# Performance work log

Measured on AMD Instinct MI355X. Metric: run time of the kernel, lower is better.

The kernel has to match this reference:

```python
import jax, jax.numpy as jnp
import numpy as np

N0, N1, N2 = 60000, 30000, 15000
E1, E2 = 960000, 480000
G, D, C = 2000, 400, 20
S0, S1, S2 = 1000, 1500, 2000  # gene index slice boundaries (shared/human/mouse)
EPS = 1e-5


def setup_inputs() -> dict:
    key = jax.random.key(0)
    ks = jax.random.split(key, 30)
    def lin(k, o, i):
        return (jax.random.normal(k, (o, i), jnp.float32) / np.sqrt(i)).astype(jnp.float32)
    inp = {}
    inp['x'] = jax.random.normal(ks[0], (N0, G), jnp.float32)
    inp['w_all'] = jax.random.uniform(ks[1], (E1 + E2, 1), jnp.float32)
    inp['W_sh'] = lin(ks[2], D, 1000); inp['b_sh'] = 0.01 * jax.random.normal(ks[3], (D,), jnp.float32)
    inp['W_hu'] = lin(ks[4], D, 500);  inp['b_hu'] = 0.01 * jax.random.normal(ks[5], (D,), jnp.float32)
    inp['W_mo'] = lin(ks[6], D, 500);  inp['b_mo'] = 0.01 * jax.random.normal(ks[7], (D,), jnp.float32)
    inp['Wn1'] = lin(ks[8], D, D);     inp['bn1'] = 0.01 * jax.random.normal(ks[9], (D,), jnp.float32)
    inp['Wn2'] = lin(ks[10], D, D);    inp['bn2'] = 0.01 * jax.random.normal(ks[11], (D,), jnp.float32)
    inp['W_lin'] = lin(ks[12], C, D);  inp['b_lin'] = 0.01 * jax.random.normal(ks[13], (C,), jnp.float32)
    inp['Wd1'] = lin(ks[14], 50, D);   inp['bd1'] = 0.01 * jax.random.normal(ks[15], (50,), jnp.float32)
    inp['gamma'] = jnp.ones((50,), jnp.float32)
    inp['beta'] = jnp.zeros((50,), jnp.float32)
    inp['Wd2'] = lin(ks[16], 2, 50);   inp['bd2'] = 0.01 * jax.random.normal(ks[17], (2,), jnp.float32)
    inp['src1'] = jax.random.randint(ks[18], (E1,), 0, N0)
    inp['dst1'] = jax.random.randint(ks[19], (E1,), 0, N1)
    inp['eid1'] = jax.random.randint(ks[20], (E1,), 0, E1 + E2)
    inp['src2'] = jax.random.randint(ks[21], (E2,), 0, N1)
    inp['dst2'] = jax.random.randint(ks[22], (E2,), 0, N2)
    inp['eid2'] = jax.random.randint(ks[23], (E2,), 0, E1 + E2)
    return inp


@jax.custom_vjp
def grad_reverse(x):
    return x

def _gr_fwd(x):
    return x, None

def _gr_bwd(_, g):
    return (-g,)  # ReverseLayerF with alpha=1

grad_reverse.defvjp(_gr_fwd, _gr_bwd)


def _gnn_layer(h_src, n_dst, src, dst, w_e, W, b):
    # weighted message gather-sum + degree-normalized self-combine (GNNConv)
    h_dst = h_src[:n_dst]
    m = h_src[src] * w_e                                   # [E, D]
    neigh = jax.ops.segment_sum(m, dst, num_segments=n_dst)
    deg = jax.ops.segment_sum(jnp.ones(dst.shape, h_src.dtype), dst, num_segments=n_dst)
    h_neigh = (neigh + h_dst) / (deg[:, None] + 1.0)
    return h_neigh @ W.T + b


def reference(x, w_all, W_sh, b_sh, W_hu, b_hu, W_mo, b_mo, Wn1, bn1, Wn2, bn2,
              W_lin, b_lin, Wd1, bd1, gamma, beta, Wd2, bd2,
              src1, dst1, eid1, src2, dst2, eid2):
    # one-hot selection matmuls == column slices of x, then three embeddings summed (FineGrainedLayerF)
    h = ((x[:, :S0] @ W_sh.T + b_sh)
         + (x[:, S0:S1] @ W_hu.T + b_hu)
         + (x[:, S1:S2] @ W_mo.T + b_mo))
    h1 = _gnn_layer(h, N1, src1, dst1, w_all[eid1], Wn1, bn1)
    h2 = _gnn_layer(h1, N2, src2, dst2, w_all[eid2], Wn2, bn2)
    h_x = h2 @ W_lin.T + b_lin
    # domain classifier on gradient-reversed features (BatchNorm1d in training mode)
    d = grad_reverse(h2) @ Wd1.T + bd1
    mu = jnp.mean(d, axis=0)
    var = jnp.var(d, axis=0)
    d = (d - mu) / jnp.sqrt(var + EPS) * gamma + beta
    d = jax.nn.relu(d)
    domain_x = d @ Wd2.T + bd2
    return (h_x, domain_x)
```

## Files before the change

### kernel.cpp

```cpp
#include <hip/hip_runtime.h>
#include <stdint.h>
#include <stddef.h>

typedef short bf16x8 __attribute__((ext_vector_type(8)));
typedef unsigned short ushort8 __attribute__((ext_vector_type(8)));
typedef unsigned short usv4 __attribute__((ext_vector_type(4)));
typedef float f32x4 __attribute__((ext_vector_type(4)));

__device__ __forceinline__ unsigned short f2bf(float f) {
  union { float f; unsigned int u; } v; v.f = f;
  unsigned int r = v.u + 0x7FFFu + ((v.u >> 16) & 1u);
  return (unsigned short)(r >> 16);
}
__device__ __forceinline__ float bf2f(unsigned short u) {
  union { unsigned int u; float f; } v; v.u = ((unsigned int)u) << 16; return v.f;
}

#define PAD 96

__global__ void prep_frag(
    const float* __restrict__ Wsh, const float* __restrict__ Whu, const float* __restrict__ Wmo,
    const float* __restrict__ Wn1, const float* __restrict__ Wn2,
    const float* __restrict__ Wlin, const float* __restrict__ Wd1,
    unsigned short* __restrict__ WCf, unsigned short* __restrict__ WN1f,
    unsigned short* __restrict__ WN2f, unsigned short* __restrict__ WHf,
    const float* __restrict__ bsh, const float* __restrict__ bhu, const float* __restrict__ bmo,
    const float* __restrict__ blin, const float* __restrict__ bd1,
    float* __restrict__ b3, float* __restrict__ bhead)
{
  const int NB_FRAG = 6784;
  const int bid = blockIdx.x;
  const int tid = threadIdx.x;
  if (bid < NB_FRAG) {
    const int s0 = 64 * 16384, s1 = s0 + 14 * 16384, s2 = s1 + 14 * 16384;
    int idx = bid * 256 + tid;
    int mode, rel;
    unsigned short* out;
    if (idx < s0)      { mode = 0; rel = idx;      out = WCf;  }
    else if (idx < s1) { mode = 1; rel = idx - s0; out = WN1f; }
    else if (idx < s2) { mode = 3; rel = idx - s1; out = WN2f; }
    else               { mode = 2; rel = idx - s2; out = WHf;  }
    int t = rel >> 14;
    int rem = rel & 16383;
    int e = rem & 7;
    int chunk = rem >> 3;
    int lane = chunk & 63;
    int g = chunk >> 6;
    int col = g * 16 + (lane & 15);
    int k = t * 32 + ((lane >> 4) << 3) + e;
    float v = 0.f;
    if (mode == 0) {
      if (col < 400 && k < 2000) {
        if (k < 1000)      v = Wsh[col * 1000 + k];
        else if (k < 1500) v = Whu[col * 500 + (k - 1000)];
        else               v = Wmo[col * 500 + (k - 1500)];
      }
    } else if (mode == 1) {
      if (col < 400 && k < 400) v = Wn1[col * 400 + k];
    } else if (mode == 3) {
      if (col < 400 && k < 400) v = Wn2[col * 400 + k];
    } else {
      if (k < 400) {
        if (col < 20)      v = Wlin[col * 400 + k];
        else if (col < 70) v = Wd1[(col - 20) * 400 + k];
      }
    }
    out[rel] = f2bf(v);
  } else {
    for (int t = tid; t < 512; t += 256) {
      if (t < 416) b3[t] = (t < 400) ? (bsh[t] + bhu[t] + bmo[t]) : 0.f;
      bhead[t] = (t < 20) ? blin[t] : ((t < 70) ? bd1[t - 20] : 0.f);
    }
  }
}

__global__ __launch_bounds__(512, 4) void gemm_stage1_adj(
    const float* __restrict__ Af, const unsigned short* __restrict__ Bf,
    const float* __restrict__ bias, unsigned short* __restrict__ C,
    int M, int Kreal, int ksteps, int NGEMM,
    const int* __restrict__ dst1, const int* __restrict__ src1, const int* __restrict__ eid1,
    int* __restrict__ cnt1, int* __restrict__ esrcP1, float* __restrict__ ewP1, int E1,
    const int* __restrict__ dst2, const int* __restrict__ src2, const int* __restrict__ eid2,
    int* __restrict__ cnt2, int* __restrict__ esrcP2, float* __restrict__ ewP2, int E2,
    const float* __restrict__ wall)
{
  __shared__ unsigned short As[2][64][36];

  if (blockIdx.x >= NGEMM) {
    int e = (blockIdx.x - NGEMM) * 512 + threadIdx.x;
    if (e < E1) {
      int d = dst1[e];
      int pos = atomicAdd(&cnt1[d], 1);
      if (pos < PAD) {
        esrcP1[d * PAD + pos] = src1[e];
        ewP1[d * PAD + pos] = wall[eid1[e]];
      }
    } else if (e < E1 + E2) {
      int e2 = e - E1;
      int d = dst2[e2];
      int pos = atomicAdd(&cnt2[d], 1);
      if (pos < PAD) {
        esrcP2[d * PAD + pos] = src2[e2];
        ewP2[d * PAD + pos] = wall[eid2[e2]];
      }
    }
    return;
  }

  const int tid = threadIdx.x;
  const int lane = tid & 63;
  const int wv = tid >> 6;
  const int rowBase = blockIdx.x * 64;
  const int sRow = tid >> 3;
  const int sC = (tid & 7) << 2;
  const int aRow = rowBase + sRow;
  const bool aOK = aRow < M;
  const int fr = lane & 15;
  const int fq = lane >> 4;

  const unsigned short* bWave = Bf + ((size_t)(wv * 4) * 64 + lane) * 8;

  f32x4 acc[4][4] = {};
  f32x4 a0, a1;
  bf16x8 bb[4];

  auto loadB = [&](int t) {
    const unsigned short* bp = bWave + (size_t)t * 16384;
    #pragma unroll
    for (int ni = 0; ni < 4; ++ni) bb[ni] = *(const bf16x8*)(bp + ni * 512);
  };
  auto loadA0 = [&](int t) {
    const int k0 = t * 32 + sC;
    if (aOK && (k0 + 4) <= Kreal) a0 = *(const f32x4*)(Af + (size_t)aRow * Kreal + k0);
    else { a0[0]=0.f; a0[1]=0.f; a0[2]=0.f; a0[3]=0.f; }
  };
  auto loadA1 = [&](int t) {
    const int k0 = t * 32 + sC;
    if (aOK && (k0 + 4) <= Kreal) a1 = *(const f32x4*)(Af + (size_t)aRow * Kreal + k0);
    else { a1[0]=0.f; a1[1]=0.f; a1[2]=0.f; a1[3]=0.f; }
  };
  auto writeA0 = [&](int buf) {
    usv4 w;
    w[0]=f2bf(a0[0]); w[1]=f2bf(a0[1]); w[2]=f2bf(a0[2]); w[3]=f2bf(a0[3]);
    *(usv4*)&As[buf][sRow][sC] = w;
  };
  auto writeA1 = [&](int buf) {
    usv4 w;
    w[0]=f2bf(a1[0]); w[1]=f2bf(a1[1]); w[2]=f2bf(a1[2]); w[3]=f2bf(a1[3]);
    *(usv4*)&As[buf][sRow][sC] = w;
  };
  auto compute = [&](int buf) {
    bf16x8 af[4];
    #pragma unroll
    for (int mi = 0; mi < 4; ++mi)
      af[mi] = *(const bf16x8*)&As[buf][(mi << 4) + fr][fq << 3];
    #pragma unroll
    for (int ni = 0; ni < 4; ++ni)
      #pragma unroll
      for (int mi = 0; mi < 4; ++mi)
        acc[mi][ni] = __builtin_amdgcn_mfma_f32_16x16x32_bf16(af[mi], bb[ni], acc[mi][ni], 0, 0, 0);
  };

  const int ksm1 = ksteps - 1;
  loadA0(0);
  loadB(0);
  loadA1(1 < ksm1 ? 1 : ksm1);
  writeA0(0);
  __syncthreads();
  loadA0(2 < ksm1 ? 2 : ksm1);

  for (int t = 0; t + 1 < ksteps; t += 2) {
    compute(0);
    loadB(t + 1);
    writeA1(1);
    __syncthreads();
    loadA1(t + 3 < ksm1 ? t + 3 : ksm1);
    compute(1);
    loadB(t + 2 < ksm1 ? t + 2 : ksm1);
    writeA0(0);
    __syncthreads();
    loadA0(t + 4 < ksm1 ? t + 4 : ksm1);
  }
  compute(0);

  #pragma unroll
  for (int mi = 0; mi < 4; ++mi) {
    const int row0 = rowBase + (mi << 4) + (fq << 2);
    #pragma unroll
    for (int ni = 0; ni < 4; ++ni) {
      const int col = (wv << 6) + (ni << 4) + fr;
      if (col < 416) {
        const float bv = (col < 400) ? bias[col] : 0.f;
        #pragma unroll
        for (int r = 0; r < 4; ++r) {
          const int row = row0 + r;
          if (row < M) C[(size_t)row * 416 + col] =
              (col < 400) ? f2bf(acc[mi][ni][r] + bv) : (unsigned short)0;
        }
      }
    }
  }
}

template<int HEAD, int ROWS>
__global__ __launch_bounds__(512) void fused_layer(
    const unsigned short* __restrict__ hsrc, const int* __restrict__ deg,
    const int* __restrict__ esrcP, const float* __restrict__ ewP,
    const unsigned short* __restrict__ Bf, const float* __restrict__ bias,
    unsigned short* __restrict__ Cout,
    const unsigned short* __restrict__ BfH, const float* __restrict__ biasH,
    float* __restrict__ outHx, float* __restrict__ dRaw, float* __restrict__ stats, int nDst)
{
  constexpr int MI = ROWS / 16;
  constexpr int NPW = ROWS / 8;
  __shared__ unsigned short T[ROWS][456];
  const int tid = threadIdx.x;
  const int lane = tid & 63;
  const int wv = tid >> 6;
  const int rowBase = blockIdx.x * ROWS;
  const int fr = lane & 15;
  const int fq = lane >> 4;

  for (int i = 0; i < NPW; ++i) {
    const int row = wv * NPW + i;
    const int node = rowBase + row;
    if (lane < 52) {
      float a[8];
      if (node < nDst) {
        ushort8 v = *(const ushort8*)(hsrc + (size_t)node * 416 + lane * 8);
        #pragma unroll
        for (int j = 0; j < 8; ++j) a[j] = bf2f(v[j]);
        int dg = deg[node]; if (dg > PAD) dg = PAD;
        const int e0 = node * PAD, e1 = e0 + dg;
        int e = e0;
        for (; e + 16 <= e1; e += 16) {
          int ss[16]; float ww[16];
          #pragma unroll
          for (int u = 0; u < 16; ++u) { ss[u] = esrcP[e + u]; ww[u] = ewP[e + u]; }
          ushort8 q0  = *(const ushort8*)(hsrc + (size_t)ss[0]  * 416 + lane * 8);
          ushort8 q1  = *(const ushort8*)(hsrc + (size_t)ss[1]  * 416 + lane * 8);
          ushort8 q2  = *(const ushort8*)(hsrc + (size_t)ss[2]  * 416 + lane * 8);
          ushort8 q3  = *(const ushort8*)(hsrc + (size_t)ss[3]  * 416 + lane * 8);
          ushort8 q4  = *(const ushort8*)(hsrc + (size_t)ss[4]  * 416 + lane * 8);
          ushort8 q5  = *(const ushort8*)(hsrc + (size_t)ss[5]  * 416 + lane * 8);
          ushort8 q6  = *(const ushort8*)(hsrc + (size_t)ss[6]  * 416 + lane * 8);
          ushort8 q7  = *(const ushort8*)(hsrc + (size_t)ss[7]  * 416 + lane * 8);
          ushort8 q8  = *(const ushort8*)(hsrc + (size_t)ss[8]  * 416 + lane * 8);
          ushort8 q9  = *(const ushort8*)(hsrc + (size_t)ss[9]  * 416 + lane * 8);
          ushort8 q10 = *(const ushort8*)(hsrc + (size_t)ss[10] * 416 + lane * 8);
          ushort8 q11 = *(const ushort8*)(hsrc + (size_t)ss[11] * 416 + lane * 8);
          ushort8 q12 = *(const ushort8*)(hsrc + (size_t)ss[12] * 416 + lane * 8);
          ushort8 q13 = *(const ushort8*)(hsrc + (size_t)ss[13] * 416 + lane * 8);
          ushort8 q14 = *(const ushort8*)(hsrc + (size_t)ss[14] * 416 + lane * 8);
          ushort8 q15 = *(const ushort8*)(hsrc + (size_t)ss[15] * 416 + lane * 8);
          #pragma unroll
          for (int j = 0; j < 8; ++j) {
            float p0 = (bf2f(q0[j])*ww[0] + bf2f(q1[j])*ww[1]) + (bf2f(q2[j])*ww[2] + bf2f(q3[j])*ww[3]);
            float p1 = (bf2f(q4[j])*ww[4] + bf2f(q5[j])*ww[5]) + (bf2f(q6[j])*ww[6] + bf2f(q7[j])*ww[7]);
            float p2 = (bf2f(q8[j])*ww[8] + bf2f(q9[j])*ww[9]) + (bf2f(q10[j])*ww[10] + bf2f(q11[j])*ww[11]);
            float p3 = (bf2f(q12[j])*ww[12] + bf2f(q13[j])*ww[13]) + (bf2f(q14[j])*ww[14] + bf2f(q15[j])*ww[15]);
            a[j] += (p0 + p1) + (p2 + p3);
          }
        }
        for (; e + 4 <= e1; e += 4) {
          const int s0 = esrcP[e], s1 = esrcP[e+1], s2 = esrcP[e+2], s3 = esrcP[e+3];
          const float w0 = ewP[e], w1 = ewP[e+1], w2 = ewP[e+2], w3 = ewP[e+3];
          ushort8 q0 = *(const ushort8*)(hsrc + (size_t)s0 * 416 + lane * 8);
          ushort8 q1 = *(const ushort8*)(hsrc + (size_t)s1 * 416 + lane * 8);
          ushort8 q2 = *(const ushort8*)(hsrc + (size_t)s2 * 416 + lane * 8);
          ushort8 q3 = *(const ushort8*)(hsrc + (size_t)s3 * 416 + lane * 8);
          #pragma unroll
          for (int j = 0; j < 8; ++j)
            a[j] += (bf2f(q0[j]) * w0 + bf2f(q1[j]) * w1) + (bf2f(q2[j]) * w2 + bf2f(q3[j]) * w3);
        }
        for (; e < e1; ++e) {
          const int s = esrcP[e];
          const float w = ewP[e];
          ushort8 q = *(const ushort8*)(hsrc + (size_t)s * 416 + lane * 8);
          #pragma unroll
          for (int j = 0; j < 8; ++j) a[j] += bf2f(q[j]) * w;
        }
        const float inv = 1.f / ((float)dg + 1.f);
        ushort8 o;
        #pragma unroll
        for (int j = 0; j < 8; ++j) o[j] = f2bf(a[j] * inv);
        *(ushort8*)&T[row][lane * 8] = o;
      } else {
        ushort8 o;
        #pragma unroll
        for (int j = 0; j < 8; ++j) o[j] = 0;
        *(ushort8*)&T[row][lane * 8] = o;
      }
    } else if (lane < 57) {
      ushort8 o;
      #pragma unroll
      for (int j = 0; j < 8; ++j) o[j] = 0;
      *(ushort8*)&T[row][416 + (lane - 52) * 8] = o;
    }
  }
  __syncthreads();

  const unsigned short* bWave = Bf + ((size_t)(wv * 4) * 64 + lane) * 8;
  f32x4 acc[MI][4] = {};
  bf16x8 bbA[4], bbB[4];

  auto loadBA = [&](int kh) {
    const unsigned short* bp = bWave + (size_t)kh * 16384;
    #pragma unroll
    for (int ni = 0; ni < 4; ++ni) bbA[ni] = *(const bf16x8*)(bp + ni * 512);
  };
  auto loadBB = [&](int kh) {
    const unsigned short* bp = bWave + (size_t)kh * 16384;
    #pragma unroll
    for (int ni = 0; ni < 4; ++ni) bbB[ni] = *(const bf16x8*)(bp + ni * 512);
  };
  auto computeA2 = [&](int kh) {
    bf16x8 af[MI];
    #pragma unroll
    for (int mi = 0; mi < MI; ++mi)
      af[mi] = *(const bf16x8*)&T[(mi << 4) + fr][kh * 32 + (fq << 3)];
    #pragma unroll
    for (int ni = 0; ni < 4; ++ni)
      #pragma unroll
      for (int mi = 0; mi < MI; ++mi)
        acc[mi][ni] = __builtin_amdgcn_mfma_f32_16x16x32_bf16(af[mi], bbA[ni], acc[mi][ni], 0, 0, 0);
  };
  auto computeB2 = [&](int kh) {
    bf16x8 af[MI];
    #pragma unroll
    for (int mi = 0; mi < MI; ++mi)
      af[mi] = *(const bf16x8*)&T[(mi << 4) + fr][kh * 32 + (fq << 3)];
    #pragma unroll
    for (int ni = 0; ni < 4; ++ni)
      #pragma unroll
      for (int mi = 0; mi < MI; ++mi)
        acc[mi][ni] = __builtin_amdgcn_mfma_f32_16x16x32_bf16(af[mi], bbB[ni], acc[mi][ni], 0, 0, 0);
  };

  loadBA(0);
  loadBB(1);
  for (int kh = 0; kh + 1 < 14; kh += 2) {
    computeA2(kh);
    loadBA(kh + 2 < 13 ? kh + 2 : 13);
    computeB2(kh + 1);
    loadBB(kh + 3 < 13 ? kh + 3 : 13);
  }

  if (HEAD == 0) {
    #pragma unroll
    for (int mi = 0; mi < MI; ++mi) {
      const int row0 = rowBase + (mi << 4) + (fq << 2);
      #pragma unroll
      for (int ni = 0; ni < 4; ++ni) {
        const int col = (wv << 6) + (ni << 4) + fr;
        if (col < 416) {
          const float bv = (col < 400) ? bias[col] : 0.f;
          #pragma unroll
          for (int r = 0; r < 4; ++r) {
            const int row = row0 + r;
            if (row < nDst) Cout[(size_t)row * 416 + col] =
                (col < 400) ? f2bf(acc[mi][ni][r] + bv) : (unsigned short)0;
          }
        }
      }
    }
  } else {
    __syncthreads();
    #pragma unroll
    for (int mi = 0; mi < MI; ++mi) {
      const int lrow0 = (mi << 4) + (fq << 2);
      #pragma unroll
      for (int ni = 0; ni < 4; ++ni) {
        const int col = (wv << 6) + (ni << 4) + fr;
        if (col < 456) {
          const float bv = (col < 400) ? bias[col] : 0.f;
          #pragma unroll
          for (int r = 0; r < 4; ++r)
            T[lrow0 + r][col] = (col < 400) ? f2bf(acc[mi][ni][r] + bv) : (unsigned short)0;
        }
      }
    }
    __syncthreads();
    const unsigned short* bhWave = BfH + ((size_t)wv * 64 + lane) * 8;
    f32x4 acc2[MI] = {};
    bf16x8 bhA, bhB;
    auto loadHA = [&](int kh) { bhA = *(const bf16x8*)(bhWave + (size_t)kh * 16384); };
    auto loadHB = [&](int kh) { bhB = *(const bf16x8*)(bhWave + (size_t)kh * 16384); };
    auto computeHA = [&](int kh) {
      #pragma unroll
      for (int mi = 0; mi < MI; ++mi) {
        bf16x8 af = *(const bf16x8*)&T[(mi << 4) + fr][kh * 32 + (fq << 3)];
        acc2[mi] = __builtin_amdgcn_mfma_f32_16x16x32_bf16(af, bhA, acc2[mi], 0, 0, 0);
      }
    };
    auto computeHB = [&](int kh) {
      #pragma unroll
      for (int mi = 0; mi < MI; ++mi) {
        bf16x8 af = *(const bf16x8*)&T[(mi << 4) + fr][kh * 32 + (fq << 3)];
        acc2[mi] = __builtin_amdgcn_mfma_f32_16x16x32_bf16(af, bhB, acc2[mi], 0, 0, 0);
      }
    };
    loadHA(0);
    loadHB(1);
    for (int kh = 0; kh + 1 < 14; kh += 2) {
      computeHA(kh);
      loadHA(kh + 2 < 13 ? kh + 2 : 13);
      computeHB(kh + 1);
      loadHB(kh + 3 < 13 ? kh + 3 : 13);
    }
    const int col = (wv << 4) + fr;
    const bool colOK = (col < 70);
    const float bv = colOK ? biasH[col] : 0.f;
    if (colOK) {
      #pragma unroll
      for (int mi = 0; mi < MI; ++mi) {
        const int row0 = rowBase + (mi << 4) + (fq << 2);
        #pragma unroll
        for (int r = 0; r < 4; ++r) {
          const int row = row0 + r;
          if (row < nDst) {
            float v = acc2[mi][r] + bv;
            if (col < 20) outHx[(size_t)row * 20 + col] = v;
            else          dRaw[(size_t)row * 50 + (col - 20)] = v;
          }
        }
      }
    }
    float s = 0.f, s2 = 0.f;
    if (col >= 20 && col < 70) {
      #pragma unroll
      for (int mi = 0; mi < MI; ++mi) {
        const int row0 = rowBase + (mi << 4) + (fq << 2);
        #pragma unroll
        for (int r = 0; r < 4; ++r) {
          if (row0 + r < nDst) {
            float v = acc2[mi][r] + bv;
            s += v; s2 += v * v;
          }
        }
      }
    }
    s  += __shfl_xor(s, 16);  s  += __shfl_xor(s, 32);
    s2 += __shfl_xor(s2, 16); s2 += __shfl_xor(s2, 32);
    if (col >= 20 && col < 70 && fq == 0) {
      atomicAdd(&stats[col - 20], s);
      atomicAdd(&stats[50 + col - 20], s2);
    }
  }
}

__global__ void domain_head2(const float* __restrict__ d, const float* __restrict__ stats,
                             const float* __restrict__ gamma, const float* __restrict__ beta,
                             const float* __restrict__ Wd2, const float* __restrict__ bd2,
                             float* __restrict__ out, int rows)
{
  __shared__ float ss[100];
  const int t = threadIdx.x;
  if (t < 50) {
    float mu = stats[t] / rows;
    float var = stats[50 + t] / rows - mu * mu;
    float inv = rsqrtf(var + 1e-5f);
    float sc = gamma[t] * inv;
    ss[t] = sc;
    ss[50 + t] = beta[t] - mu * sc;
  }
  __syncthreads();
  int r = blockIdx.x * 256 + t;
  if (r >= rows) return;
  float o0 = bd2[0], o1 = bd2[1];
  const float* dr = d + (size_t)r * 50;
  #pragma unroll 10
  for (int c = 0; c < 50; ++c) {
    float v = dr[c] * ss[c] + ss[50 + c];
    v = fmaxf(v, 0.f);
    o0 += v * Wd2[c];
    o1 += v * Wd2[50 + c];
  }
  out[r * 2]     = o0;
  out[r * 2 + 1] = o1;
}

extern "C" void kernel_launch(void* const* d_in, const int* in_sizes, int n_in,
                              void* d_out, int out_size, void* d_ws, size_t ws_size,
                              hipStream_t stream)
{
  const float* x    = (const float*)d_in[0];
  const float* wall = (const float*)d_in[1];
  const float* Wsh  = (const float*)d_in[2];
  const float* bsh  = (const float*)d_in[3];
  const float* Whu  = (const float*)d_in[4];
  const float* bhu  = (const float*)d_in[5];
  const float* Wmo  = (const float*)d_in[6];
  const float* bmo  = (const float*)d_in[7];
  const float* Wn1  = (const float*)d_in[8];
  const float* bn1  = (const float*)d_in[9];
  const float* Wn2  = (const float*)d_in[10];
  const float* bn2  = (const float*)d_in[11];
  const float* Wlin = (const float*)d_in[12];
  const float* blin = (const float*)d_in[13];
  const float* Wd1  = (const float*)d_in[14];
  const float* bd1  = (const float*)d_in[15];
  const float* gamma= (const float*)d_in[16];
  const float* beta = (const float*)d_in[17];
  const float* Wd2  = (const float*)d_in[18];
  const float* bd2  = (const float*)d_in[19];
  const int* src1 = (const int*)d_in[20];
  const int* dst1 = (const int*)d_in[21];
  const int* eid1 = (const int*)d_in[22];
  const int* src2 = (const int*)d_in[23];
  const int* dst2 = (const int*)d_in[24];
  const int* eid2 = (const int*)d_in[25];

  char* ws = (char*)d_ws;
  unsigned short* h    = (unsigned short*)(ws);
  unsigned short* h1   = (unsigned short*)(ws + 49920000ULL);
  float* d_raw         = (float*)(ws + 74880000ULL);
  unsigned short* WCf  = (unsigned short*)(ws + 77880000ULL);
  unsigned short* WN1f = (unsigned short*)(ws + 79977152ULL);
  unsigned short* WN2f = (unsigned short*)(ws + 80435904ULL);
  unsigned short* WHf  = (unsigned short*)(ws + 80894656ULL);
  float* b3      = (float*)(ws + 81353408ULL);
  float* bhead   = (float*)(ws + 81355456ULL);
  int*   cnt1    = (int*)(ws + 81357504ULL);
  int*   cnt2    = (int*)(ws + 81477504ULL);
  float* stats   = (float*)(ws + 81537504ULL);
  int*   esrcP1  = (int*)(ws + 81538304ULL);
  float* ewP1    = (float*)(ws + 93058304ULL);
  int*   esrcP2  = (int*)(ws + 104578304ULL);
  float* ewP2    = (float*)(ws + 110338304ULL);

  const int E1 = 960000, E2 = 480000;
  const int N0 = 60000, N1 = 30000, N2 = 15000;

  (void)hipMemsetAsync(cnt1, 0, 180400, stream);

  prep_frag<<<6785, 256, 0, stream>>>(
      Wsh, Whu, Wmo, Wn1, Wn2, Wlin, Wd1, WCf, WN1f, WN2f, WHf,
      bsh, bhu, bmo, blin, bd1, b3, bhead);

  gemm_stage1_adj<<<938 + 2813, 512, 0, stream>>>(
      x, WCf, b3, h, N0, 2000, 63, 938,
      dst1, src1, eid1, cnt1, esrcP1, ewP1, E1,
      dst2, src2, eid2, cnt2, esrcP2, ewP2, E2, wall);

  float* out_hx  = (float*)d_out;
  float* out_dom = (float*)d_out + 300000;

  fused_layer<0, 32><<<(N1 + 31) / 32, 512, 0, stream>>>(
      h, cnt1, esrcP1, ewP1, WN1f, bn1, h1, nullptr, nullptr, nullptr, nullptr, nullptr, N1);

  fused_layer<1, 32><<<(N2 + 31) / 32, 512, 0, stream>>>(
      h1, cnt2, esrcP2, ewP2, WN2f, bn2, nullptr, WHf, bhead, out_hx, d_raw, stats, N2);

  domain_head2<<<(N2 + 255) / 256, 256, 0, stream>>>(d_raw, stats, gamma, beta, Wd2, bd2, out_dom, N2);
}
```

Measured before the change: 500.4 us.

## Load A fragments directly into registers and split GEMM columns across two blocks

The stage-1 GEMM no longer stages the fp32 A tile through shared memory with barriers. Each wave now loads its own A fragments straight from global memory and converts them with packed bf16 conversion instructions. Blocks shrink to 256 threads, each covering half the output columns, so twice as many blocks share each row tile and the adjacency-bucketing part of the grid is resized to match. This removes LDS traffic and __syncthreads, but every wave now reads the full A row tile itself, so global/L2 reads of x are duplicated across the 8 column groups.

```diff
diff --git a/kernel.cpp b/kernel.cpp
--- a/kernel.cpp
+++ b/kernel.cpp
@@ -4,7 +4,6 @@
 
 typedef short bf16x8 __attribute__((ext_vector_type(8)));
 typedef unsigned short ushort8 __attribute__((ext_vector_type(8)));
-typedef unsigned short usv4 __attribute__((ext_vector_type(4)));
 typedef float f32x4 __attribute__((ext_vector_type(4)));
 
 __device__ __forceinline__ unsigned short f2bf(float f) {
@@ -14,6 +13,16 @@
 }
 __device__ __forceinline__ float bf2f(unsigned short u) {
   union { unsigned int u; float f; } v; v.u = ((unsigned int)u) << 16; return v.f;
+}
+__device__ __forceinline__ bf16x8 cvt8(f32x4 lo, f32x4 hi) {
+  unsigned int r0, r1, r2, r3;
+  asm("v_cvt_pk_bf16_f32 %0, %1, %2" : "=v"(r0) : "v"(lo[0]), "v"(lo[1]));
+  asm("v_cvt_pk_bf16_f32 %0, %1, %2" : "=v"(r1) : "v"(lo[2]), "v"(lo[3]));
+  asm("v_cvt_pk_bf16_f32 %0, %1, %2" : "=v"(r2) : "v"(hi[0]), "v"(hi[1]));
+  asm("v_cvt_pk_bf16_f32 %0, %1, %2" : "=v"(r3) : "v"(hi[2]), "v"(hi[3]));
+  union { unsigned int u[4]; bf16x8 v; } z;
+  z.u[0] = r0; z.u[1] = r1; z.u[2] = r2; z.u[3] = r3;
+  return z.v;
 }
 
 #define PAD 96
@@ -74,7 +83,7 @@
   }
 }
 
-__global__ __launch_bounds__(512, 4) void gemm_stage1_adj(
+__global__ __launch_bounds__(256, 2) void gemm_stage1_adj(
     const float* __restrict__ Af, const unsigned short* __restrict__ Bf,
     const float* __restrict__ bias, unsigned short* __restrict__ C,
     int M, int Kreal, int ksteps, int NGEMM,
@@ -84,10 +93,8 @@
     int* __restrict__ cnt2, int* __restrict__ esrcP2, float* __restrict__ ewP2, int E2,
     const float* __restrict__ wall)
 {
-  __shared__ unsigned short As[2][64][36];
-
   if (blockIdx.x >= NGEMM) {
-    int e = (blockIdx.x - NGEMM) * 512 + threadIdx.x;
+    int e = (blockIdx.x - NGEMM) * 256 + threadIdx.x;
     if (e < E1) {
       int d = dst1[e];
       int pos = atomicAdd(&cnt1[d], 1);
@@ -110,85 +117,99 @@
   const int tid = threadIdx.x;
   const int lane = tid & 63;
   const int wv = tid >> 6;
-  const int rowBase = blockIdx.x * 64;
-  const int sRow = tid >> 3;
-  const int sC = (tid & 7) << 2;
-  const int aRow = rowBase + sRow;
-  const bool aOK = aRow < M;
+  const int colgrp = ((blockIdx.x & 1) << 2) + wv;
+  const int rowBase = (blockIdx.x >> 1) * 64;
   const int fr = lane & 15;
   const int fq = lane >> 4;
 
-  const unsigned short* bWave = Bf + ((size_t)(wv * 4) * 64 + lane) * 8;
+  const unsigned short* bWave = Bf + ((size_t)(colgrp * 4) * 64 + lane) * 8;
+  const float* aRowP[4];
+  #pragma unroll
+  for (int mi = 0; mi < 4; ++mi) {
+    int row = rowBase + (mi << 4) + fr;
+    if (row >= M) row = M - 1;
+    aRowP[mi] = Af + (size_t)row * Kreal + (fq << 3);
+  }
 
   f32x4 acc[4][4] = {};
-  f32x4 a0, a1;
-  bf16x8 bb[4];
-
-  auto loadB = [&](int t) {
+  f32x4 a0lo[4], a0hi[4], a1lo[4], a1hi[4];
+  bf16x8 bb0[4], bb1[4];
+
+  auto loadB0 = [&](int t) {
     const unsigned short* bp = bWave + (size_t)t * 16384;
     #pragma unroll
-    for (int ni = 0; ni < 4; ++ni) bb[ni] = *(const bf16x8*)(bp + ni * 512);
+    for (int ni = 0; ni < 4; ++ni) bb0[ni] = *(const bf16x8*)(bp + ni * 512);
+  };
+  auto loadB1 = [&](int t) {
+    const unsigned short* bp = bWave + (size_t)t * 16384;
+    #pragma unroll
+    for (int ni = 0; ni < 4; ++ni) bb1[ni] = *(const bf16x8*)(bp + ni * 512);
   };
   auto loadA0 = [&](int t) {
-    const int k0 = t * 32 + sC;
-    if (aOK && (k0 + 4) <= Kreal) a0 = *(const f32x4*)(Af + (size_t)aRow * Kreal + k0);
-    else { a0[0]=0.f; a0[1]=0.f; a0[2]=0.f; a0[3]=0.f; }
+    const int k0 = t * 32;
+    const bool kOK = (k0 + (fq << 3) + 8) <= Kreal;
+    #pragma unroll
+    for (int mi = 0; mi < 4; ++mi) {
+      if (kOK) {
+        a0lo[mi] = *(const f32x4*)(aRowP[mi] + k0);
+        a0hi[mi] = *(const f32x4*)(aRowP[mi] + k0 + 4);
+      } else {
+        a0lo[mi][0]=0.f; a0lo[mi][1]=0.f; a0lo[mi][2]=0.f; a0lo[mi][3]=0.f;
+        a0hi[mi][0]=0.f; a0hi[mi][1]=0.f; a0hi[mi][2]=0.f; a0hi[mi][3]=0.f;
+      }
+    }
   };
   auto loadA1 = [&](int t) {
-    const int k0 = t * 32 + sC;
-    if (aOK && (k0 + 4) <= Kreal) a1 = *(const f32x4*)(Af + (size_t)aRow * Kreal + k0);
-    else { a1[0]=0.f; a1[1]=0.f; a1[2]=0.f; a1[3]=0.f; }
-  };
-  auto writeA0 = [&](int buf) {
-    usv4 w;
-    w[0]=f2bf(a0[0]); w[1]=f2bf(a0[1]); w[2]=f2bf(a0[2]); w[3]=f2bf(a0[3]);
-    *(usv4*)&As[buf][sRow][sC] = w;
-  };
-  auto writeA1 = [&](int buf) {
-    usv4 w;
-    w[0]=f2bf(a1[0]); w[1]=f2bf(a1[1]); w[2]=f2bf(a1[2]); w[3]=f2bf(a1[3]);
-    *(usv4*)&As[buf][sRow][sC] = w;
-  };
-  auto compute = [&](int buf) {
-    bf16x8 af[4];
-    #pragma unroll
-    for (int mi = 0; mi < 4; ++mi)
-      af[mi] = *(const bf16x8*)&As[buf][(mi << 4) + fr][fq << 3];
-    #pragma unroll
-    for (int ni = 0; ni < 4; ++ni)
-      #pragma unroll
-      for (int mi = 0; mi < 4; ++mi)
-        acc[mi][ni] = __builtin_amdgcn_mfma_f32_16x16x32_bf16(af[mi], bb[ni], acc[mi][ni], 0, 0, 0);
-  };
-
-  const int ksm1 = ksteps - 1;
+    const int k0 = t * 32;
+    const bool kOK = (k0 + (fq << 3) + 8) <= Kreal;
+    #pragma unroll
+    for (int mi = 0; mi < 4; ++mi) {
+      if (kOK) {
+        a1lo[mi] = *(const f32x4*)(aRowP[mi] + k0);
+        a1hi[mi] = *(const f32x4*)(aRowP[mi] + k0 + 4);
+      } else {
+        a1lo[mi][0]=0.f; a1lo[mi][1]=0.f; a1lo[mi][2]=0.f; a1lo[mi][3]=0.f;
+        a1hi[mi][0]=0.f; a1hi[mi][1]=0.f; a1hi[mi][2]=0.f; a1hi[mi][3]=0.f;
+      }
+    }
+  };
+  auto compute0 = [&]() {
+    #pragma unroll
+    for (int mi = 0; mi < 4; ++mi) {
+      bf16x8 af = cvt8(a0lo[mi], a0hi[mi]);
+      #pragma unroll
+      for (int ni = 0; ni < 4; ++ni)
+        acc[mi][ni] = __builtin_amdgcn_mfma_f32_16x16x32_bf16(af, bb0[ni], acc[mi][ni], 0, 0, 0);
+    }
+  };
+  auto compute1 = [&]() {
+    #pragma unroll
+    for (int mi = 0; mi < 4; ++mi) {
+      bf16x8 af = cvt8(a1lo[mi], a1hi[mi]);
+      #pragma unroll
+      for (int ni = 0; ni < 4; ++ni)
+        acc[mi][ni] = __builtin_amdgcn_mfma_f32_16x16x32_bf16(af, bb1[ni], acc[mi][ni], 0, 0, 0);
+    }
+  };
+
   loadA0(0);
-  loadB(0);
-  loadA1(1 < ksm1 ? 1 : ksm1);
-  writeA0(0);
-  __syncthreads();
-  loadA0(2 < ksm1 ? 2 : ksm1);
-
+  loadB0(0);
   for (int t = 0; t + 1 < ksteps; t += 2) {
-    compute(0);
-    loadB(t + 1);
-    writeA1(1);
-    __syncthreads();
-    loadA1(t + 3 < ksm1 ? t + 3 : ksm1);
-    compute(1);
-    loadB(t + 2 < ksm1 ? t + 2 : ksm1);
-    writeA0(0);
-    __syncthreads();
-    loadA0(t + 4 < ksm1 ? t + 4 : ksm1);
-  }
-  compute(0);
+    loadA1(t + 1);
+    loadB1(t + 1);
+    compute0();
+    loadA0(t + 2);
+    loadB0(t + 2);
+    compute1();
+  }
+  compute0();
 
   #pragma unroll
   for (int mi = 0; mi < 4; ++mi) {
     const int row0 = rowBase + (mi << 4) + (fq << 2);
     #pragma unroll
     for (int ni = 0; ni < 4; ++ni) {
-      const int col = (wv << 6) + (ni << 4) + fr;
+      const int col = (colgrp << 6) + (ni << 4) + fr;
       if (col < 416) {
         const float bv = (col < 400) ? bias[col] : 0.f;
         #pragma unroll
@@ -538,8 +559,8 @@
       Wsh, Whu, Wmo, Wn1, Wn2, Wlin, Wd1, WCf, WN1f, WN2f, WHf,
       bsh, bhu, bmo, blin, bd1, b3, bhead);
 
-  gemm_stage1_adj<<<938 + 2813, 512, 0, stream>>>(
-      x, WCf, b3, h, N0, 2000, 63, 938,
+  gemm_stage1_adj<<<1876 + 5625, 256, 0, stream>>>(
+      x, WCf, b3, h, N0, 2000, 63, 1876,
       dst1, src1, eid1, cnt1, esrcP1, ewP1, E1,
       dst2, src2, eid2, cnt2, esrcP2, ewP2, E2, wall);
 
```

Result: slower. 761.8 us (+52.3%).
